# Kernel tuning notes

Hardware: AMD Instinct MI355X
Metric: run time of the kernel (lower is better)

Reference implementation:

```python
import jax, jax.numpy as jnp
import numpy as np

B, N, F, O = 4, 4096, 64, 64


def setup_inputs() -> dict:
    key = jax.random.key(0)
    k0, k1, k2, k3, k4 = jax.random.split(key, 5)
    x = jax.random.normal(k0, (B, N, F), dtype=jnp.float32)
    # adj_transform: Linear(2F -> 1): weight (2F,), bias scalar
    adj_w = jax.random.normal(k1, (2 * F,), dtype=jnp.float32) * (1.0 / np.sqrt(2 * F))
    adj_b = jax.random.normal(k2, (), dtype=jnp.float32)
    # GCN weight: xavier_normal_ over (F, O)
    weight = jax.random.normal(k3, (F, O), dtype=jnp.float32) * np.sqrt(2.0 / (F + O))
    bias = jax.random.normal(k4, (O,), dtype=jnp.float32)
    return {"x": x, "adj_w": adj_w, "adj_b": adj_b, "weight": weight, "bias": bias}


def reference(x, adj_w, adj_b, weight, bias):
    f = x.shape[-1]
    # Original: tmp[b,i,j] = x[b,j]; adj[b,i,j] = Linear(cat(x[b,j], x[b,i]))
    # = x[b,j]\u00b7adj_w[:F] + x[b,i]\u00b7adj_w[F:] + adj_b  (exact decomposition,
    # avoids materializing the (B,N,N,2F) concat tensor)
    s_col = jnp.einsum('bnf,f->bn', x, adj_w[:f])   # contributes along j
    s_row = jnp.einsum('bnf,f->bn', x, adj_w[f:])   # contributes along i
    adj = s_row[:, :, None] + s_col[:, None, :] + adj_b  # (B, N, N)
    # symmetric degree normalization with clamp(min=1)
    deg_inv_sqrt = jnp.clip(adj.sum(axis=-1), 1.0, None) ** -0.5  # (B, N)
    adj = deg_inv_sqrt[:, :, None] * adj * deg_inv_sqrt[:, None, :]
    out = jnp.einsum('bij,bjo->bio', adj, x @ weight) + bias
    return jax.nn.relu(out)
```

## Files before the change

kernel.cpp:

```cpp
#include <hip/hip_runtime.h>

#define Bq 4
#define Nq 4096
#define Fq 64
#define Oq 64


__global__ __launch_bounds__(256) void k1_rowdots(
    const float* __restrict__ x, const float* __restrict__ adj_w,
    float* __restrict__ s_row, float* __restrict__ s_col,
    float* __restrict__ blocksum) {
  int r = blockIdx.x * 256 + threadIdx.x;
  const float4* xr = reinterpret_cast<const float4*>(x + (size_t)r * Fq);
  const float4* w0 = reinterpret_cast<const float4*>(adj_w);
  const float4* w1 = reinterpret_cast<const float4*>(adj_w + Fq);
  float sc = 0.f, sr = 0.f;
#pragma unroll
  for (int k = 0; k < Fq / 4; ++k) {
    float4 v = xr[k];
    float4 a = w0[k];
    float4 b = w1[k];
    sc += v.x * a.x + v.y * a.y + v.z * a.z + v.w * a.w;
    sr += v.x * b.x + v.y * b.y + v.z * b.z + v.w * b.w;
  }
  s_col[r] = sc;
  s_row[r] = sr;
  __shared__ float red[256];
  red[threadIdx.x] = sc;
  __syncthreads();
  for (int s = 128; s > 0; s >>= 1) {
    if (threadIdx.x < s) red[threadIdx.x] += red[threadIdx.x + s];
    __syncthreads();
  }
  if (threadIdx.x == 0) blocksum[blockIdx.x] = red[0];
}

__global__ __launch_bounds__(256) void k2_weighted(
    const float* __restrict__ x, const float* __restrict__ s_row,
    const float* __restrict__ s_col, const float* __restrict__ blocksum,
    const float* __restrict__ adj_bp, float* __restrict__ pxd,
    float* __restrict__ pxsd) {
  int b = blockIdx.x >> 5;
  int chunk = blockIdx.x & 31;
  int f = threadIdx.x & 63;
  int jsub = threadIdx.x >> 6;
  const float adj_b = adj_bp[0];
  float scs = 0.f;
#pragma unroll
  for (int k = 0; k < 16; ++k) scs += blocksum[b * 16 + k];
  const int jcnt = Nq / 32;
  int j0 = chunk * jcnt;
  float axd = 0.f, axsd = 0.f;
  for (int j = j0 + jsub; j < j0 + jcnt; j += 4) {
    int row = b * Nq + j;
    float srj = s_row[row];
    float scj = s_col[row];
    float rowsum = fmaf((float)Nq, srj + adj_b, scs);
    float dj = rsqrtf(fmaxf(rowsum, 1.0f));
    float xv = x[(size_t)row * Fq + f];
    axd = fmaf(dj, xv, axd);
    axsd = fmaf(scj * dj, xv, axsd);
  }
  __shared__ float red[2][4][64];
  red[0][jsub][f] = axd;
  red[1][jsub][f] = axsd;
  __syncthreads();
  if (threadIdx.x < 64) {
    pxd[blockIdx.x * 64 + f] =
        red[0][0][f] + red[0][1][f] + red[0][2][f] + red[0][3][f];
  } else if (threadIdx.x < 128) {
    pxsd[blockIdx.x * 64 + f] =
        red[1][0][f] + red[1][1][f] + red[1][2][f] + red[1][3][f];
  }
}

__global__ __launch_bounds__(256) void k3_out(
    const float* __restrict__ s_row, const float* __restrict__ blocksum,
    const float* __restrict__ adj_bp, const float* __restrict__ pxd,
    const float* __restrict__ pxsd, const float* __restrict__ weight,
    const float* __restrict__ bias, float* __restrict__ out) {
  int b = blockIdx.x >> 6;
  int ibase = (blockIdx.x & 63) << 6;
  const float adj_b = adj_bp[0];
  float scs = 0.f;
#pragma unroll
  for (int k = 0; k < 16; ++k) scs += blocksum[b * 16 + k];
  __shared__ float xdl[64], xsdl[64], u[64], v[64];
  int t = threadIdx.x;
  if (t < 128) {
    int f = t & 63;
    const float* p = ((t < 64) ? pxd : pxsd) + (size_t)(b * 32) * 64 + f;
    float a = 0.f;
#pragma unroll
    for (int c = 0; c < 32; ++c) a += p[c * 64];
    if (t < 64)
      xdl[f] = a;
    else
      xsdl[f] = a;
  }
  __syncthreads();
  if (t < 128) {
    int o = t & 63;
    const float* src = (t < 64) ? xdl : xsdl;
    float acc = 0.f;
#pragma unroll
    for (int f = 0; f < Fq; ++f) acc = fmaf(src[f], weight[f * Oq + o], acc);
    if (t < 64)
      u[o] = acc;
    else
      v[o] = acc;
  }
  __syncthreads();
  int o0 = (t & 15) * 4;
#pragma unroll
  for (int pass = 0; pass < 4; ++pass) {
    int row = ibase + pass * 16 + (t >> 4);
    int rg = b * Nq + row;
    float sr = s_row[rg];
    float rowsum = fmaf((float)Nq, sr + adj_b, scs);
    float di = rsqrtf(fmaxf(rowsum, 1.0f));
    float a = di * (sr + adj_b);
    float4 r;
    r.x = fmaxf(0.f, fmaf(a, u[o0 + 0], fmaf(di, v[o0 + 0], bias[o0 + 0])));
    r.y = fmaxf(0.f, fmaf(a, u[o0 + 1], fmaf(di, v[o0 + 1], bias[o0 + 1])));
    r.z = fmaxf(0.f, fmaf(a, u[o0 + 2], fmaf(di, v[o0 + 2], bias[o0 + 2])));
    r.w = fmaxf(0.f, fmaf(a, u[o0 + 3], fmaf(di, v[o0 + 3], bias[o0 + 3])));
    reinterpret_cast<float4*>(out + (size_t)rg * Oq)[t & 15] = r;
  }
}

extern "C" void kernel_launch(void* const* d_in, const int* in_sizes, int n_in,
                              void* d_out, int out_size, void* d_ws,
                              size_t ws_size, hipStream_t stream) {
  const float* x = (const float*)d_in[0];
  const float* adj_w = (const float*)d_in[1];
  const float* adj_b = (const float*)d_in[2];
  const float* weight = (const float*)d_in[3];
  const float* bias = (const float*)d_in[4];
  float* out = (float*)d_out;

  float* ws = (float*)d_ws;
  float* s_row = ws;
  float* s_col = ws + Bq * Nq;
  float* blocksum = ws + 2 * Bq * Nq;
  float* pxd = blocksum + 64;
  float* pxsd = pxd + 128 * 64;

  k1_rowdots<<<64, 256, 0, stream>>>(x, adj_w, s_row, s_col, blocksum);
  k2_weighted<<<Bq * 32, 256, 0, stream>>>(x, s_row, s_col, blocksum, adj_b,
                                           pxd, pxsd);
  k3_out<<<256, 256, 0, stream>>>(s_row, blocksum, adj_b, pxd, pxsd, weight,
                                  bias, out);
}
```

Baseline: 78.12 us.

## Fuse three GCN kernels into one cooperative kernel with grid syncs

Replaces the three separate launches (row dots, weighted reductions, output) with a single cooperative kernel of 64 blocks that uses grid.sync between phases. Each block keeps its own 256 rows across all phases, so x rows and s_row/s_col are reused with better locality. The aim is to remove launch overhead and inter-kernel gaps. In exchange, parallelism in the later phases drops to 64 blocks, and cooperative launch plus grid barriers add their own cost.

```diff
diff --git a/kernel.cpp b/kernel.cpp
--- a/kernel.cpp
+++ b/kernel.cpp
@@ -1,131 +1,126 @@
 #include <hip/hip_runtime.h>
+#include <hip/hip_cooperative_groups.h>
+
+namespace cg = cooperative_groups;
 
 #define Bq 4
 #define Nq 4096
 #define Fq 64
 #define Oq 64
 
+__global__ __launch_bounds__(256) void gcn_fused(
+    const float* __restrict__ x, const float* __restrict__ adj_w,
+    const float* __restrict__ adj_bp, const float* __restrict__ weight,
+    const float* __restrict__ bias, float* __restrict__ out,
+    float* __restrict__ ws) {
+  float* s_row = ws;
+  float* s_col = ws + Bq * Nq;
+  float* blocksum = ws + 2 * Bq * Nq;
+  float* pxd = blocksum + 64;
+  float* pxsd = pxd + 64 * 64;
 
-__global__ __launch_bounds__(256) void k1_rowdots(
-    const float* __restrict__ x, const float* __restrict__ adj_w,
-    float* __restrict__ s_row, float* __restrict__ s_col,
-    float* __restrict__ blocksum) {
-  int r = blockIdx.x * 256 + threadIdx.x;
-  const float4* xr = reinterpret_cast<const float4*>(x + (size_t)r * Fq);
-  const float4* w0 = reinterpret_cast<const float4*>(adj_w);
-  const float4* w1 = reinterpret_cast<const float4*>(adj_w + Fq);
-  float sc = 0.f, sr = 0.f;
+  cg::grid_group grid = cg::this_grid();
+  const int k = blockIdx.x;
+  const int t = threadIdx.x;
+  const int b = k >> 4;
+  const float adj_b = adj_bp[0];
+
+  __shared__ float red[2][4][64];
+  __shared__ float uv[4][64];
+
+  {
+    int r = k * 256 + t;
+    const float4* xr = reinterpret_cast<const float4*>(x + (size_t)r * Fq);
+    const float4* w0 = reinterpret_cast<const float4*>(adj_w);
+    const float4* w1 = reinterpret_cast<const float4*>(adj_w + Fq);
+    float sc = 0.f, sr = 0.f;
 #pragma unroll
-  for (int k = 0; k < Fq / 4; ++k) {
-    float4 v = xr[k];
-    float4 a = w0[k];
-    float4 b = w1[k];
-    sc += v.x * a.x + v.y * a.y + v.z * a.z + v.w * a.w;
-    sr += v.x * b.x + v.y * b.y + v.z * b.z + v.w * b.w;
+    for (int q = 0; q < Fq / 4; ++q) {
+      float4 v = xr[q];
+      float4 a = w0[q];
+      float4 c = w1[q];
+      sc += v.x * a.x + v.y * a.y + v.z * a.z + v.w * a.w;
+      sr += v.x * c.x + v.y * c.y + v.z * c.z + v.w * c.w;
+    }
+    s_col[r] = sc;
+    s_row[r] = sr;
+    float* redf = &red[0][0][0];
+    redf[t] = sc;
+    __syncthreads();
+    for (int s = 128; s > 0; s >>= 1) {
+      if (t < s) redf[t] += redf[t + s];
+      __syncthreads();
+    }
+    if (t == 0) blocksum[k] = redf[0];
   }
-  s_col[r] = sc;
-  s_row[r] = sr;
-  __shared__ float red[256];
-  red[threadIdx.x] = sc;
-  __syncthreads();
-  for (int s = 128; s > 0; s >>= 1) {
-    if (threadIdx.x < s) red[threadIdx.x] += red[threadIdx.x + s];
-    __syncthreads();
-  }
-  if (threadIdx.x == 0) blocksum[blockIdx.x] = red[0];
-}
+  __threadfence();
+  grid.sync();
 
-__global__ __launch_bounds__(256) void k2_weighted(
-    const float* __restrict__ x, const float* __restrict__ s_row,
-    const float* __restrict__ s_col, const float* __restrict__ blocksum,
-    const float* __restrict__ adj_bp, float* __restrict__ pxd,
-    float* __restrict__ pxsd) {
-  int b = blockIdx.x >> 5;
-  int chunk = blockIdx.x & 31;
-  int f = threadIdx.x & 63;
-  int jsub = threadIdx.x >> 6;
-  const float adj_b = adj_bp[0];
   float scs = 0.f;
 #pragma unroll
-  for (int k = 0; k < 16; ++k) scs += blocksum[b * 16 + k];
-  const int jcnt = Nq / 32;
-  int j0 = chunk * jcnt;
-  float axd = 0.f, axsd = 0.f;
-  for (int j = j0 + jsub; j < j0 + jcnt; j += 4) {
-    int row = b * Nq + j;
-    float srj = s_row[row];
-    float scj = s_col[row];
-    float rowsum = fmaf((float)Nq, srj + adj_b, scs);
-    float dj = rsqrtf(fmaxf(rowsum, 1.0f));
-    float xv = x[(size_t)row * Fq + f];
-    axd = fmaf(dj, xv, axd);
-    axsd = fmaf(scj * dj, xv, axsd);
+  for (int c = 0; c < 16; ++c) scs += blocksum[b * 16 + c];
+  {
+    int f = t & 63;
+    int jsub = t >> 6;
+    float axd = 0.f, axsd = 0.f;
+    int row0 = k * 256;
+    for (int j = jsub; j < 256; j += 4) {
+      int row = row0 + j;
+      float srj = s_row[row];
+      float scj = s_col[row];
+      float dj = rsqrtf(fmaxf(fmaf((float)Nq, srj + adj_b, scs), 1.0f));
+      float xv = x[(size_t)row * Fq + f];
+      axd = fmaf(dj, xv, axd);
+      axsd = fmaf(scj * dj, xv, axsd);
+    }
+    __syncthreads();
+    red[0][jsub][f] = axd;
+    red[1][jsub][f] = axsd;
+    __syncthreads();
+    if (t < 64) {
+      pxd[k * 64 + f] = red[0][0][f] + red[0][1][f] + red[0][2][f] + red[0][3][f];
+    } else if (t < 128) {
+      pxsd[k * 64 + f] = red[1][0][f] + red[1][1][f] + red[1][2][f] + red[1][3][f];
+    }
   }
-  __shared__ float red[2][4][64];
-  red[0][jsub][f] = axd;
-  red[1][jsub][f] = axsd;
-  __syncthreads();
-  if (threadIdx.x < 64) {
-    pxd[blockIdx.x * 64 + f] =
-        red[0][0][f] + red[0][1][f] + red[0][2][f] + red[0][3][f];
-  } else if (threadIdx.x < 128) {
-    pxsd[blockIdx.x * 64 + f] =
-        red[1][0][f] + red[1][1][f] + red[1][2][f] + red[1][3][f];
-  }
-}
+  __threadfence();
+  grid.sync();
 
-__global__ __launch_bounds__(256) void k3_out(
-    const float* __restrict__ s_row, const float* __restrict__ blocksum,
-    const float* __restrict__ adj_bp, const float* __restrict__ pxd,
-    const float* __restrict__ pxsd, const float* __restrict__ weight,
-    const float* __restrict__ bias, float* __restrict__ out) {
-  int b = blockIdx.x >> 6;
-  int ibase = (blockIdx.x & 63) << 6;
-  const float adj_b = adj_bp[0];
-  float scs = 0.f;
-#pragma unroll
-  for (int k = 0; k < 16; ++k) scs += blocksum[b * 16 + k];
-  __shared__ float xdl[64], xsdl[64], u[64], v[64];
-  int t = threadIdx.x;
   if (t < 128) {
     int f = t & 63;
-    const float* p = ((t < 64) ? pxd : pxsd) + (size_t)(b * 32) * 64 + f;
+    const float* p = ((t < 64) ? pxd : pxsd) + (size_t)(b * 16) * 64 + f;
     float a = 0.f;
 #pragma unroll
-    for (int c = 0; c < 32; ++c) a += p[c * 64];
-    if (t < 64)
-      xdl[f] = a;
-    else
-      xsdl[f] = a;
+    for (int c = 0; c < 16; ++c) a += p[c * 64];
+    uv[(t < 64) ? 0 : 1][f] = a;
   }
   __syncthreads();
   if (t < 128) {
     int o = t & 63;
-    const float* src = (t < 64) ? xdl : xsdl;
+    const float* src = uv[(t < 64) ? 0 : 1];
     float acc = 0.f;
 #pragma unroll
     for (int f = 0; f < Fq; ++f) acc = fmaf(src[f], weight[f * Oq + o], acc);
-    if (t < 64)
-      u[o] = acc;
-    else
-      v[o] = acc;
+    uv[(t < 64) ? 2 : 3][o] = acc;
   }
   __syncthreads();
-  int o0 = (t & 15) * 4;
+  {
+    int o0 = (t & 15) * 4;
+    const float* u = uv[2];
+    const float* v = uv[3];
 #pragma unroll
-  for (int pass = 0; pass < 4; ++pass) {
-    int row = ibase + pass * 16 + (t >> 4);
-    int rg = b * Nq + row;
-    float sr = s_row[rg];
-    float rowsum = fmaf((float)Nq, sr + adj_b, scs);
-    float di = rsqrtf(fmaxf(rowsum, 1.0f));
-    float a = di * (sr + adj_b);
-    float4 r;
-    r.x = fmaxf(0.f, fmaf(a, u[o0 + 0], fmaf(di, v[o0 + 0], bias[o0 + 0])));
-    r.y = fmaxf(0.f, fmaf(a, u[o0 + 1], fmaf(di, v[o0 + 1], bias[o0 + 1])));
-    r.z = fmaxf(0.f, fmaf(a, u[o0 + 2], fmaf(di, v[o0 + 2], bias[o0 + 2])));
-    r.w = fmaxf(0.f, fmaf(a, u[o0 + 3], fmaf(di, v[o0 + 3], bias[o0 + 3])));
-    reinterpret_cast<float4*>(out + (size_t)rg * Oq)[t & 15] = r;
+    for (int pass = 0; pass < 16; ++pass) {
+      int row = k * 256 + pass * 16 + (t >> 4);
+      float sr = s_row[row];
+      float di = rsqrtf(fmaxf(fmaf((float)Nq, sr + adj_b, scs), 1.0f));
+      float a = di * (sr + adj_b);
+      float4 r;
+      r.x = fmaxf(0.f, fmaf(a, u[o0 + 0], fmaf(di, v[o0 + 0], bias[o0 + 0])));
+      r.y = fmaxf(0.f, fmaf(a, u[o0 + 1], fmaf(di, v[o0 + 1], bias[o0 + 1])));
+      r.z = fmaxf(0.f, fmaf(a, u[o0 + 2], fmaf(di, v[o0 + 2], bias[o0 + 2])));
+      r.w = fmaxf(0.f, fmaf(a, u[o0 + 3], fmaf(di, v[o0 + 3], bias[o0 + 3])));
+      reinterpret_cast<float4*>(out + (size_t)row * Oq)[t & 15] = r;
+    }
   }
 }
 
@@ -138,17 +133,10 @@
   const float* weight = (const float*)d_in[3];
   const float* bias = (const float*)d_in[4];
   float* out = (float*)d_out;
+  float* ws = (float*)d_ws;
 
-  float* ws = (float*)d_ws;
-  float* s_row = ws;
-  float* s_col = ws + Bq * Nq;
-  float* blocksum = ws + 2 * Bq * Nq;
-  float* pxd = blocksum + 64;
-  float* pxsd = pxd + 128 * 64;
-
-  k1_rowdots<<<64, 256, 0, stream>>>(x, adj_w, s_row, s_col, blocksum);
-  k2_weighted<<<Bq * 32, 256, 0, stream>>>(x, s_row, s_col, blocksum, adj_b,
-                                           pxd, pxsd);
-  k3_out<<<256, 256, 0, stream>>>(s_row, blocksum, adj_b, pxd, pxsd, weight,
-                                  bias, out);
+  void* args[] = {(void*)&x,      (void*)&adj_w, (void*)&adj_b, (void*)&weight,
+                  (void*)&bias,   (void*)&out,   (void*)&ws};
+  hipLaunchCooperativeKernel((void*)gcn_fused, dim3(64), dim3(256), args, 0,
+                             stream);
 }
```

New measurement: 122.6 us. 1.57x slower.
